# Performance work log

Hardware: AMD Instinct MI355X
Metric: run time of the kernel (lower is better)

The kernel has to match this reference:

```python
import jax, jax.numpy as jnp
import numpy as np

DIM = 128      # size_in
SIGN = 4       # number of leading outputs negated
CONST = 0.618  # additive constant in Linear_v5
BATCH = 4096


def setup_inputs() -> dict:
    key = jax.random.key(0)
    k0, k1, k2, k3, k4 = jax.random.split(key, 5)
    s1 = 1.0 / np.sqrt(DIM)
    s2 = 1.0 / np.sqrt(2 * DIM)
    return {
        "t": 0,
        "input_": jax.random.normal(k0, (BATCH, 2 * DIM), dtype=jnp.float32),
        "W1": jax.random.uniform(k1, (2 * DIM, DIM), jnp.float32, -s1, s1),
        "b1": jax.random.uniform(k2, (2 * DIM,), jnp.float32, -s1, s1),
        "W2": jax.random.uniform(k3, (DIM, 2 * DIM), jnp.float32, -s2, s2),
        "b2": jax.random.uniform(k4, (DIM,), jnp.float32, -s2, s2),
    }


def reference(t, input_, W1, b1, W2, b2):
    x = input_[:, :DIM]   # [B, D]
    v = input_[:, DIM:]   # [B, D]
    dtype = x.dtype
    # sign vector: first SIGN outputs of g are negated (applied after sigmoid+const)
    sgn = jnp.where(jnp.arange(DIM) < SIGN, -1.0, 1.0).astype(dtype)  # [D]

    h = x @ W1.T + b1                      # [B, 2D]
    a = jax.nn.relu(h)
    s = jax.nn.sigmoid(a @ W2.T + b2)      # [B, D]
    g = sgn * (s + CONST)                  # [B, D]

    # Analytic batch Jacobian J[b,i,j] = d g_i / d x_j
    # = sgn_i * s_i(1-s_i) * sum_k W2[i,k] * 1[h_bk>0] * W1[k,j]
    mask = (h > 0).astype(dtype)           # [B, 2D]
    Jcore = jnp.einsum('ik,bk,kj->bij', W2, mask, W1)   # [B, D, D]
    J = (sgn * (s * (1.0 - s)))[:, :, None] * Jcore      # [B, D, D]

    g_inv = 1.0 / g                        # [B, D]
    conn1 = -J * g_inv[:, None, :]         # [B, i, j] * g_inv_j
    conn2 = J * g_inv[:, :, None]          # [B, i, j] * g_inv_i

    dv_vec = v[:, :, None] * v[:, None, :]               # [B, i, j] = v_i v_j
    vtemp1 = jnp.sum((v * v)[:, :, None] * conn1, axis=1)  # sum_i v_i^2 conn1[b,i,j]
    vtemp2 = jnp.einsum('bji,bji->bj', dv_vec, conn2)
    vtemp3 = jnp.einsum('bij,bji->bj', dv_vec, conn2)
    dv = vtemp1 + vtemp2 + vtemp3          # [B, D]

    return jnp.concatenate([v, dv], axis=1)  # [B, 2D]
```

## Files before the change

kernel.cpp:

```cpp
#include <hip/hip_runtime.h>
#include <math.h>

#define DIM    128
#define DIM2   256
#define NSIGN  4
#define CCONST 0.618f
#define MB     16
#define NTHR   512

typedef short bf16x8 __attribute__((ext_vector_type(8)));
typedef float f32x4  __attribute__((ext_vector_type(4)));

#define MFMA(a,b,c) __builtin_amdgcn_mfma_f32_16x16x32_bf16((a),(b),(c),0,0,0)

union BU { uint4 q; bf16x8 b; };

__device__ __forceinline__ unsigned short f2bf(float f) {
    unsigned u = __float_as_uint(f);
    u += 0x7fffu + ((u >> 16) & 1u);
    return (unsigned short)(u >> 16);
}
__device__ __forceinline__ float bf2f(unsigned short h) {
    return __uint_as_float(((unsigned)h) << 16);
}
__device__ __forceinline__ bf16x8 frag16(const unsigned short* p) {
    BU u; u.q = *(const uint4*)p; return u.b;
}

__global__ void prep_pack(const float* __restrict__ W1, const float* __restrict__ W2,
                          unsigned short* __restrict__ pk) {
    int tid  = blockIdx.x * 256 + threadIdx.x;
    int m    = tid >> 12;
    int f    = tid & 4095;
    int lane = f & 63;
    int tkt  = f >> 6;
    int r0   = ((tkt & ((m == 0 || m == 2) ? 3 : 7)) * 32) + ((lane >> 4) << 3);
    int nt   = tkt / ((m == 0 || m == 2) ? 4 : 8);
    int c    = nt * 16 + (lane & 15);

    union { uint4 q; unsigned short u[8]; } H, L;
    #pragma unroll
    for (int e = 0; e < 8; ++e) {
        int r = r0 + e;
        float v;
        if      (m == 0) v = W1[c * DIM  + r];
        else if (m == 1) v = W2[c * DIM2 + r];
        else if (m == 2) v = W2[r * DIM2 + c];
        else             v = W1[r * DIM  + c];
        unsigned short hb = f2bf(v);
        H.u[e] = hb;
        L.u[e] = f2bf(v - bf2f(hb));
    }
    size_t base = (size_t)m * 65536 + (size_t)(tkt * 64 + lane) * 8;
    *(uint4*)(pk + base) = H.q;
    if (m == 0) *(uint4*)(pk + base + 32768) = L.q;
}

__global__ __launch_bounds__(NTHR, 1)
void fused_connection(const float* __restrict__ input_,
                      const float* __restrict__ b1,
                      const float* __restrict__ b2,
                      const unsigned short* __restrict__ pk,
                      float* __restrict__ out) {
    __shared__ __align__(16) float          vv [MB][132];
    __shared__ __align__(16) unsigned short xbH[MB][136];
    __shared__ __align__(16) unsigned short xbL[MB][136];
    __shared__ __align__(16) unsigned short vbH[MB][136];
    __shared__ __align__(16) unsigned short aH [MB][264];
    __shared__ __align__(16) unsigned short mwH[MB][264];
    __shared__ __align__(16) unsigned short vcH[MB][136];

    const int t    = threadIdx.x;
    const int lane = t & 63;
    const int w    = t >> 6;
    const int b0   = blockIdx.x * MB;
    const int arow = lane & 15;
    const int kg   = (lane >> 4) << 3;
    const int rbase = (lane >> 4) << 2;

    uint4 b1hq[2][4], b1lq[2][4];
    #pragma unroll
    for (int nt2 = 0; nt2 < 2; ++nt2)
        #pragma unroll
        for (int kt = 0; kt < 4; ++kt) {
            const unsigned short* bp = pk + (size_t)((((w * 2 + nt2) * 4 + kt) * 64 + lane) * 8);
            b1hq[nt2][kt] = *(const uint4*)bp;
            b1lq[nt2][kt] = *(const uint4*)(bp + 32768);
        }

    {
        int prow = t >> 5;
        int pc   = (t & 31) * 8;
        const float4* src = (const float4*)(input_ + (size_t)(b0 + prow) * DIM2 + pc);
        float4 f0 = src[0], f1 = src[1];
        float fa[8] = {f0.x, f0.y, f0.z, f0.w, f1.x, f1.y, f1.z, f1.w};
        if (pc < DIM) {
            union { unsigned short u[8]; uint4 q; } H, L;
            #pragma unroll
            for (int e = 0; e < 8; ++e) {
                unsigned short hb = f2bf(fa[e]);
                H.u[e] = hb;
                L.u[e] = f2bf(fa[e] - bf2f(hb));
            }
            *(uint4*)&xbH[prow][pc] = H.q;
            *(uint4*)&xbL[prow][pc] = L.q;
        } else {
            int c = pc - DIM;
            *(float4*)&vv[prow][c]     = f0;
            *(float4*)&vv[prow][c + 4] = f1;
            union { unsigned short u[8]; uint4 q; } H;
            #pragma unroll
            for (int e = 0; e < 8; ++e) H.u[e] = f2bf(fa[e]);
            *(uint4*)&vbH[prow][c] = H.q;
            float4* op = (float4*)(out + (size_t)(b0 + prow) * DIM2 + c);
            op[0] = f0; op[1] = f1;
        }
    }
    __syncthreads();

    uint4 b2q[8];
    {
        const unsigned short* p1 = pk + 65536;
        #pragma unroll
        for (int kt = 0; kt < 8; ++kt)
            b2q[kt] = *(const uint4*)(p1 + (size_t)((w * 8 + kt) * 64 + lane) * 8);

        bf16x8 xH[4], xL[4], vH[4];
        #pragma unroll
        for (int kt = 0; kt < 4; ++kt) {
            int k0 = kt * 32 + kg;
            xH[kt] = frag16(&xbH[arow][k0]);
            xL[kt] = frag16(&xbL[arow][k0]);
            vH[kt] = frag16(&vbH[arow][k0]);
        }
        #pragma unroll
        for (int nt2 = 0; nt2 < 2; ++nt2) {
            int nt = w * 2 + nt2;
            f32x4 ha = {0.f, 0.f, 0.f, 0.f};
            f32x4 wa = {0.f, 0.f, 0.f, 0.f};
            #pragma unroll
            for (int kt = 0; kt < 4; ++kt) {
                BU bh, bl;
                bh.q = b1hq[nt2][kt];
                bl.q = b1lq[nt2][kt];
                ha = MFMA(xH[kt], bh.b, ha);
                ha = MFMA(xH[kt], bl.b, ha);
                ha = MFMA(xL[kt], bh.b, ha);
                wa = MFMA(vH[kt], bh.b, wa);
            }
            int col  = nt * 16 + arow;
            float bias = b1[col];
            #pragma unroll
            for (int reg = 0; reg < 4; ++reg) {
                int row = rbase + reg;
                float hv = ha[reg] + bias;
                bool  mk = hv > 0.f;
                aH[row][col]  = f2bf(mk ? hv : 0.f);
                mwH[row][col] = f2bf(mk ? wa[reg] : 0.f);
            }
        }
    }
    __syncthreads();

    float sreg[4];
    f32x4 t2a = {0.f, 0.f, 0.f, 0.f};
    uint4 b3q[2][4];
    {
        const unsigned short* p2 = pk + 2 * 65536;
        #pragma unroll
        for (int nt2 = 0; nt2 < 2; ++nt2)
            #pragma unroll
            for (int kt = 0; kt < 4; ++kt)
                b3q[nt2][kt] = *(const uint4*)(p2 + (size_t)((((w * 2 + nt2) * 4 + kt) * 64 + lane) * 8));

        f32x4 za = {0.f, 0.f, 0.f, 0.f};
        #pragma unroll
        for (int kt = 0; kt < 8; ++kt) {
            int k0 = kt * 32 + kg;
            bf16x8 af = frag16(&aH[arow][k0]);
            bf16x8 mf = frag16(&mwH[arow][k0]);
            BU bh; bh.q = b2q[kt];
            za  = MFMA(af, bh.b, za);
            t2a = MFMA(mf, bh.b, t2a);
        }
        int   ci   = w * 16 + arow;
        float sg_i = (ci < NSIGN) ? -1.f : 1.f;
        float b2v  = b2[ci];
        #pragma unroll
        for (int reg = 0; reg < 4; ++reg) {
            int row = rbase + reg;
            float z = za[reg] + b2v;
            float s = 1.f / (1.f + __expf(-z));
            sreg[reg] = s;
            float vvl = vv[row][ci];
            vcH[row][ci] = f2bf(vvl * vvl * sg_i * s * (1.f - s));
        }
    }
    __syncthreads();

    uint4 b4q[8];
    {
        const unsigned short* p3 = pk + 3 * 65536;
        #pragma unroll
        for (int kt = 0; kt < 8; ++kt)
            b4q[kt] = *(const uint4*)(p3 + (size_t)((w * 8 + kt) * 64 + lane) * 8);

        bf16x8 cH[4];
        #pragma unroll
        for (int kt = 0; kt < 4; ++kt)
            cH[kt] = frag16(&vcH[arow][kt * 32 + kg]);
        #pragma unroll
        for (int nt2 = 0; nt2 < 2; ++nt2) {
            int nt = w * 2 + nt2;
            f32x4 ua = {0.f, 0.f, 0.f, 0.f};
            #pragma unroll
            for (int kt = 0; kt < 4; ++kt) {
                BU bh; bh.q = b3q[nt2][kt];
                ua = MFMA(cH[kt], bh.b, ua);
            }
            int ck = nt * 16 + arow;
            #pragma unroll
            for (int reg = 0; reg < 4; ++reg) {
                int row = rbase + reg;
                bool mk = aH[row][ck] != 0;
                mwH[row][ck] = f2bf(mk ? ua[reg] : 0.f);
            }
        }
    }
    __syncthreads();

    {
        f32x4 t1a = {0.f, 0.f, 0.f, 0.f};
        #pragma unroll
        for (int kt = 0; kt < 8; ++kt) {
            bf16x8 mf = frag16(&mwH[arow][kt * 32 + kg]);
            BU bh; bh.q = b4q[kt];
            t1a = MFMA(mf, bh.b, t1a);
        }
        int   cj   = w * 16 + arow;
        float sg_j = (cj < NSIGN) ? -1.f : 1.f;
        #pragma unroll
        for (int reg = 0; reg < 4; ++reg) {
            int row = rbase + reg;
            float s  = sreg[reg];
            float cv = sg_j * s * (1.f - s);
            float gi = 1.f / (sg_j * (s + CCONST));
            float vvl = vv[row][cj];
            float dv = fmaf(-gi, t1a[reg], 2.f * vvl * gi * cv * t2a[reg]);
            out[(size_t)(b0 + row) * DIM2 + DIM + cj] = dv;
        }
    }
}

extern "C" void kernel_launch(void* const* d_in, const int* in_sizes, int n_in,
                              void* d_out, int out_size, void* d_ws, size_t ws_size,
                              hipStream_t stream) {
    const float* input_ = (const float*)d_in[1];
    const float* W1 = (const float*)d_in[2];
    const float* b1 = (const float*)d_in[3];
    const float* W2 = (const float*)d_in[4];
    const float* b2 = (const float*)d_in[5];
    float* out = (float*)d_out;
    unsigned short* pk = (unsigned short*)d_ws;

    const int batch = in_sizes[1] / DIM2;

    prep_pack<<<64, 256, 0, stream>>>(W1, W2, pk);
    fused_connection<<<batch / MB, NTHR, 0, stream>>>(input_, b1, b2, pk, out);
}
```

Before: 16.71 us.

## Double block to 1024 threads, one N-tile per wave, load weights per stage

The block grows from 8 to 16 waves. In the 256-wide stages each wave now owns a single 16-column tile, while in the 128-wide stages only the first 8 waves work. Weight fragments are no longer prefetched into registers ahead of time; they are loaded from global memory inside each stage. The goal is more waves in flight and lower register pressure, at the cost of half the waves sitting idle in two stages and weight-load latency landing on the critical path.

Measured after the change: 18.00 us. 1.08x slower.

```diff
diff --git a/kernel.cpp b/kernel.cpp
--- a/kernel.cpp
+++ b/kernel.cpp
@@ -6,7 +6,7 @@
 #define NSIGN  4
 #define CCONST 0.618f
 #define MB     16
-#define NTHR   512
+#define NTHR   1024
 
 typedef short bf16x8 __attribute__((ext_vector_type(8)));
 typedef float f32x4  __attribute__((ext_vector_type(4)));
@@ -56,7 +56,7 @@
     if (m == 0) *(uint4*)(pk + base + 32768) = L.q;
 }
 
-__global__ __launch_bounds__(NTHR, 1)
+__global__ __launch_bounds__(NTHR)
 void fused_connection(const float* __restrict__ input_,
                       const float* __restrict__ b1,
                       const float* __restrict__ b2,
@@ -78,114 +78,89 @@
     const int kg   = (lane >> 4) << 3;
     const int rbase = (lane >> 4) << 2;
 
-    uint4 b1hq[2][4], b1lq[2][4];
+    uint4 b1hq[4], b1lq[4];
     #pragma unroll
-    for (int nt2 = 0; nt2 < 2; ++nt2)
-        #pragma unroll
-        for (int kt = 0; kt < 4; ++kt) {
-            const unsigned short* bp = pk + (size_t)((((w * 2 + nt2) * 4 + kt) * 64 + lane) * 8);
-            b1hq[nt2][kt] = *(const uint4*)bp;
-            b1lq[nt2][kt] = *(const uint4*)(bp + 32768);
-        }
+    for (int kt = 0; kt < 4; ++kt) {
+        const unsigned short* bp = pk + (size_t)(((w * 4 + kt) * 64 + lane) * 8);
+        b1hq[kt] = *(const uint4*)bp;
+        b1lq[kt] = *(const uint4*)(bp + 32768);
+    }
+    const float b1v = b1[w * 16 + arow];
+    float b2v = 0.f;
+    if (w < 8) b2v = b2[w * 16 + arow];
 
     {
-        int prow = t >> 5;
-        int pc   = (t & 31) * 8;
-        const float4* src = (const float4*)(input_ + (size_t)(b0 + prow) * DIM2 + pc);
-        float4 f0 = src[0], f1 = src[1];
-        float fa[8] = {f0.x, f0.y, f0.z, f0.w, f1.x, f1.y, f1.z, f1.w};
+        int prow = t >> 6;
+        int pc   = (t & 63) * 4;
+        const float4 f = *(const float4*)(input_ + (size_t)(b0 + prow) * DIM2 + pc);
+        float fa[4] = {f.x, f.y, f.z, f.w};
         if (pc < DIM) {
-            union { unsigned short u[8]; uint4 q; } H, L;
+            union { unsigned short u[4]; ushort4 q; } H, L;
             #pragma unroll
-            for (int e = 0; e < 8; ++e) {
+            for (int e = 0; e < 4; ++e) {
                 unsigned short hb = f2bf(fa[e]);
                 H.u[e] = hb;
                 L.u[e] = f2bf(fa[e] - bf2f(hb));
             }
-            *(uint4*)&xbH[prow][pc] = H.q;
-            *(uint4*)&xbL[prow][pc] = L.q;
+            *(ushort4*)&xbH[prow][pc] = H.q;
+            *(ushort4*)&xbL[prow][pc] = L.q;
         } else {
             int c = pc - DIM;
-            *(float4*)&vv[prow][c]     = f0;
-            *(float4*)&vv[prow][c + 4] = f1;
-            union { unsigned short u[8]; uint4 q; } H;
+            *(float4*)&vv[prow][c] = f;
+            union { unsigned short u[4]; ushort4 q; } H;
             #pragma unroll
-            for (int e = 0; e < 8; ++e) H.u[e] = f2bf(fa[e]);
-            *(uint4*)&vbH[prow][c] = H.q;
-            float4* op = (float4*)(out + (size_t)(b0 + prow) * DIM2 + c);
-            op[0] = f0; op[1] = f1;
-        }
-    }
-    __syncthreads();
-
-    uint4 b2q[8];
+            for (int e = 0; e < 4; ++e) H.u[e] = f2bf(fa[e]);
+            *(ushort4*)&vbH[prow][c] = H.q;
+            *(float4*)(out + (size_t)(b0 + prow) * DIM2 + c) = f;
+        }
+    }
+    __syncthreads();
+
     {
-        const unsigned short* p1 = pk + 65536;
-        #pragma unroll
-        for (int kt = 0; kt < 8; ++kt)
-            b2q[kt] = *(const uint4*)(p1 + (size_t)((w * 8 + kt) * 64 + lane) * 8);
-
-        bf16x8 xH[4], xL[4], vH[4];
+        f32x4 ha = {0.f, 0.f, 0.f, 0.f};
+        f32x4 wa = {0.f, 0.f, 0.f, 0.f};
         #pragma unroll
         for (int kt = 0; kt < 4; ++kt) {
             int k0 = kt * 32 + kg;
-            xH[kt] = frag16(&xbH[arow][k0]);
-            xL[kt] = frag16(&xbL[arow][k0]);
-            vH[kt] = frag16(&vbH[arow][k0]);
-        }
-        #pragma unroll
-        for (int nt2 = 0; nt2 < 2; ++nt2) {
-            int nt = w * 2 + nt2;
-            f32x4 ha = {0.f, 0.f, 0.f, 0.f};
-            f32x4 wa = {0.f, 0.f, 0.f, 0.f};
-            #pragma unroll
-            for (int kt = 0; kt < 4; ++kt) {
-                BU bh, bl;
-                bh.q = b1hq[nt2][kt];
-                bl.q = b1lq[nt2][kt];
-                ha = MFMA(xH[kt], bh.b, ha);
-                ha = MFMA(xH[kt], bl.b, ha);
-                ha = MFMA(xL[kt], bh.b, ha);
-                wa = MFMA(vH[kt], bh.b, wa);
-            }
-            int col  = nt * 16 + arow;
-            float bias = b1[col];
-            #pragma unroll
-            for (int reg = 0; reg < 4; ++reg) {
-                int row = rbase + reg;
-                float hv = ha[reg] + bias;
-                bool  mk = hv > 0.f;
-                aH[row][col]  = f2bf(mk ? hv : 0.f);
-                mwH[row][col] = f2bf(mk ? wa[reg] : 0.f);
-            }
+            bf16x8 xH = frag16(&xbH[arow][k0]);
+            bf16x8 xL = frag16(&xbL[arow][k0]);
+            bf16x8 vH = frag16(&vbH[arow][k0]);
+            BU bh, bl;
+            bh.q = b1hq[kt];
+            bl.q = b1lq[kt];
+            ha = MFMA(xH, bh.b, ha);
+            ha = MFMA(xH, bl.b, ha);
+            ha = MFMA(xL, bh.b, ha);
+            wa = MFMA(vH, bh.b, wa);
+        }
+        int col = w * 16 + arow;
+        #pragma unroll
+        for (int reg = 0; reg < 4; ++reg) {
+            int row = rbase + reg;
+            float hv = ha[reg] + b1v;
+            bool  mk = hv > 0.f;
+            aH[row][col]  = f2bf(mk ? hv : 0.f);
+            mwH[row][col] = f2bf(mk ? wa[reg] : 0.f);
         }
     }
     __syncthreads();
 
     float sreg[4];
     f32x4 t2a = {0.f, 0.f, 0.f, 0.f};
-    uint4 b3q[2][4];
-    {
-        const unsigned short* p2 = pk + 2 * 65536;
-        #pragma unroll
-        for (int nt2 = 0; nt2 < 2; ++nt2)
-            #pragma unroll
-            for (int kt = 0; kt < 4; ++kt)
-                b3q[nt2][kt] = *(const uint4*)(p2 + (size_t)((((w * 2 + nt2) * 4 + kt) * 64 + lane) * 8));
-
+    if (w < 8) {
+        const unsigned short* p1 = pk + 65536;
         f32x4 za = {0.f, 0.f, 0.f, 0.f};
         #pragma unroll
         for (int kt = 0; kt < 8; ++kt) {
             int k0 = kt * 32 + kg;
             bf16x8 af = frag16(&aH[arow][k0]);
             bf16x8 mf = frag16(&mwH[arow][k0]);
-            BU bh; bh.q = b2q[kt];
+            BU bh; bh.q = *(const uint4*)(p1 + (size_t)((w * 8 + kt) * 64 + lane) * 8);
             za  = MFMA(af, bh.b, za);
             t2a = MFMA(mf, bh.b, t2a);
         }
         int   ci   = w * 16 + arow;
         float sg_i = (ci < NSIGN) ? -1.f : 1.f;
-        float b2v  = b2[ci];
         #pragma unroll
         for (int reg = 0; reg < 4; ++reg) {
             int row = rbase + reg;
@@ -198,43 +173,32 @@
     }
     __syncthreads();
 
-    uint4 b4q[8];
     {
+        const unsigned short* p2 = pk + 2 * 65536;
+        f32x4 ua = {0.f, 0.f, 0.f, 0.f};
+        #pragma unroll
+        for (int kt = 0; kt < 4; ++kt) {
+            bf16x8 cH = frag16(&vcH[arow][kt * 32 + kg]);
+            BU bh; bh.q = *(const uint4*)(p2 + (size_t)(((w * 4 + kt) * 64 + lane) * 8));
+            ua = MFMA(cH, bh.b, ua);
+        }
+        int ck = w * 16 + arow;
+        #pragma unroll
+        for (int reg = 0; reg < 4; ++reg) {
+            int row = rbase + reg;
+            bool mk = aH[row][ck] != 0;
+            mwH[row][ck] = f2bf(mk ? ua[reg] : 0.f);
+        }
+    }
+    __syncthreads();
+
+    if (w < 8) {
         const unsigned short* p3 = pk + 3 * 65536;
-        #pragma unroll
-        for (int kt = 0; kt < 8; ++kt)
-            b4q[kt] = *(const uint4*)(p3 + (size_t)((w * 8 + kt) * 64 + lane) * 8);
-
-        bf16x8 cH[4];
-        #pragma unroll
-        for (int kt = 0; kt < 4; ++kt)
-            cH[kt] = frag16(&vcH[arow][kt * 32 + kg]);
-        #pragma unroll
-        for (int nt2 = 0; nt2 < 2; ++nt2) {
-            int nt = w * 2 + nt2;
-            f32x4 ua = {0.f, 0.f, 0.f, 0.f};
-            #pragma unroll
-            for (int kt = 0; kt < 4; ++kt) {
-                BU bh; bh.q = b3q[nt2][kt];
-                ua = MFMA(cH[kt], bh.b, ua);
-            }
-            int ck = nt * 16 + arow;
-            #pragma unroll
-            for (int reg = 0; reg < 4; ++reg) {
-                int row = rbase + reg;
-                bool mk = aH[row][ck] != 0;
-                mwH[row][ck] = f2bf(mk ? ua[reg] : 0.f);
-            }
-        }
-    }
-    __syncthreads();
-
-    {
         f32x4 t1a = {0.f, 0.f, 0.f, 0.f};
         #pragma unroll
         for (int kt = 0; kt < 8; ++kt) {
             bf16x8 mf = frag16(&mwH[arow][kt * 32 + kg]);
-            BU bh; bh.q = b4q[kt];
+            BU bh; bh.q = *(const uint4*)(p3 + (size_t)((w * 8 + kt) * 64 + lane) * 8);
             t1a = MFMA(mf, bh.b, t1a);
         }
         int   cj   = w * 16 + arow;
```
